# Optimization experiments

Hardware: AMD Instinct MI355X
Metric: run time of the kernel (lower is better)

The kernel has to match this reference:

```python
import jax, jax.numpy as jnp
import numpy as np

DIM = 768
N_IMGS = 1024
N_PATCH = 196
GRID = int(np.sqrt(N_PATCH))  # 14
B = 64


def setup_inputs() -> dict:
    key = jax.random.key(0)
    ks = jax.random.split(key, 12)
    x = jax.random.normal(ks[0], (B, N_PATCH, DIM), dtype=jnp.float32)
    mask = jnp.ones((B, N_PATCH), dtype=jnp.bool_)
    img_ids = jax.random.randint(ks[1], (B,), 0, N_IMGS, dtype=jnp.int32)
    eps = jax.random.normal(ks[2], (B, 2, N_PATCH), dtype=jnp.float32)
    s = 0.02
    Wq = jax.random.normal(ks[3], (DIM, DIM), dtype=jnp.float32) * s
    bq = jnp.zeros((DIM,), dtype=jnp.float32)
    Wk = jax.random.normal(ks[4], (DIM, DIM), dtype=jnp.float32) * s
    bk = jnp.zeros((DIM,), dtype=jnp.float32)
    Wv = jax.random.normal(ks[5], (DIM, DIM), dtype=jnp.float32) * s
    bv = jnp.zeros((DIM,), dtype=jnp.float32)
    # per-image Gaussian location params: means in [0, GRID-1], small positive stds
    avgs = jax.random.uniform(ks[6], (N_IMGS, 2, N_PATCH), dtype=jnp.float32) * (GRID - 1)
    std_devs = jax.random.uniform(ks[7], (N_IMGS, 2, N_PATCH), dtype=jnp.float32) * 1.5 + 0.1
    return {"x": x, "mask": mask, "img_ids": img_ids, "eps": eps,
            "Wq": Wq, "bq": bq, "Wk": Wk, "bk": bk, "Wv": Wv, "bv": bv,
            "avgs": avgs, "std_devs": std_devs}


def reference(x, mask, img_ids, eps, Wq, bq, Wk, bk, Wv, bv, avgs, std_devs):
    # projections: (B,S,D)
    q = jnp.einsum('bsd,ed->bse', x, Wq) + bq
    k = jnp.einsum('bsd,ed->bse', x, Wk) + bk
    v = jnp.einsum('bsd,ed->bse', x, Wv) + bv

    # sample per-query key coordinates: torch.normal(mean, std) == mean + std * eps
    mu = avgs[img_ids]        # (B,2,S)
    sd = std_devs[img_ids]    # (B,2,S)
    coord = mu + sd * eps     # (B,2,S)
    kx, ky = coord[:, 0], coord[:, 1]           # each (B,S)
    kx1, kx2 = jnp.ceil(kx), jnp.floor(kx)
    ky1, ky2 = jnp.ceil(ky), jnp.floor(ky)

    # 4 interpolation-corner flat indices per query: grid*y + x  -> (B,S,4)
    idx = jnp.stack([GRID * ky1 + kx1,
                     GRID * ky1 + kx2,
                     GRID * ky2 + kx1,
                     GRID * ky2 + kx2], axis=-1)
    idx = jnp.clip(idx, 0, N_PATCH - 1).astype(jnp.int32)

    bidx = jnp.arange(idx.shape[0])[:, None, None]  # (B,1,1)
    sampled_k = k[bidx, idx]  # (B,S,4,D)
    sampled_v = v[bidx, idx]  # (B,S,4,D)

    # softmax over the 4 sampled keys (elementwise per feature), weighted sum of values
    w = jax.nn.softmax(q[:, :, None, :] * sampled_k, axis=2)  # (B,S,4,D)
    out = jnp.sum(w * sampled_v, axis=2)                      # (B,S,D)
    return out
```

## Files before the change

### kernel.cpp

```cpp
#include <hip/hip_runtime.h>
#include <hip/hip_bf16.h>

typedef _Float16 f16;
typedef f16 f16x4 __attribute__((ext_vector_type(4)));
typedef f16 f16x8 __attribute__((ext_vector_type(8)));
typedef float f32x4 __attribute__((ext_vector_type(4)));

#define DIM   768
#define NP    196
#define BATCH 64
#define MROWS (BATCH * NP)
#define NCOLS (3 * DIM)
#define GRIDF 14.0f

#define NX4   (MROWS * DIM / 4)
#define NW4   (DIM * DIM / 4)
#define NB4   (NCOLS / 4)
#define NCVTA (NX4 + 3 * NW4 + NB4)

__global__ __launch_bounds__(256) void convert_inputs(
    const float* __restrict__ x,
    const float* __restrict__ Wq, const float* __restrict__ Wk, const float* __restrict__ Wv,
    const float* __restrict__ bq, const float* __restrict__ bk, const float* __restrict__ bv,
    f16* __restrict__ x_h, f16* __restrict__ W_h, float* __restrict__ bias_all) {
  int i = blockIdx.x * 256 + threadIdx.x;
  if (i >= NCVTA) return;
  if (i < NX4 + 3 * NW4) {
    const float* src;
    f16* dst;
    int j;
    if (i < NX4) { src = x; dst = x_h; j = i; }
    else {
      j = i - NX4;
      if (j < NW4)          { src = Wq; dst = W_h; }
      else if (j < 2 * NW4) { src = Wk; dst = W_h + DIM * DIM;     j -= NW4; }
      else                  { src = Wv; dst = W_h + 2 * DIM * DIM; j -= 2 * NW4; }
    }
    float4 v = ((const float4*)src)[j];
    f16x4 h;
    h[0] = (f16)v.x; h[1] = (f16)v.y; h[2] = (f16)v.z; h[3] = (f16)v.w;
    ((f16x4*)dst)[j] = h;
  } else {
    int j = i - (NX4 + 3 * NW4);
    float4 v = (j < 192) ? ((const float4*)bq)[j]
             : (j < 384) ? ((const float4*)bk)[j - 192]
                         : ((const float4*)bv)[j - 384];
    ((float4*)bias_all)[j] = v;
  }
}

#define BM 128
#define BN 128
#define BK 64
#define NT (DIM / BK)

__device__ __forceinline__ void gl_lds16(const f16* g, f16* l) {
  __builtin_amdgcn_global_load_lds(
      (const __attribute__((address_space(1))) void*)g,
      (__attribute__((address_space(3))) void*)l, 16, 0, 0);
}

#define MFMA16(acc_, av, bv) acc_ = __builtin_amdgcn_mfma_f32_16x16x32_f16(av, bv, acc_, 0, 0, 0)
#define BAR    __builtin_amdgcn_s_barrier()
#define LGKM8  asm volatile("s_waitcnt lgkmcnt(8)" ::: "memory")
#define LGKM0  asm volatile("s_waitcnt lgkmcnt(0)" ::: "memory")
#define VMCNT8 asm volatile("s_waitcnt vmcnt(8)" ::: "memory")
#define VMCNT0 asm volatile("s_waitcnt vmcnt(0)" ::: "memory")

#define sAoff(buf) ((buf) * (BM * BK))
#define sBoff(buf) (2 * BM * BK + (buf) * (BN * BK))

__global__ __launch_bounds__(256, 2) void gemm_qkv(
    const f16* __restrict__ A, const f16* __restrict__ W,
    const float* __restrict__ bias_all, f16* __restrict__ C) {
  __shared__ __align__(16) f16 lds[4 * BM * BK];

  const int t    = threadIdx.x;
  const int lane = t & 63;
  const int wid  = t >> 6;
  const int wr   = wid >> 1;
  const int wc   = wid & 1;

  const int nwg = 98 * 18, qq = nwg / 8, rr = nwg % 8;
  const int xcd = blockIdx.x & 7, seq = blockIdx.x >> 3;
  const int logical = (xcd < rr ? xcd * (qq + 1) : rr * (qq + 1) + (xcd - rr) * qq) + seq;
  const int bm0 = (logical / 18) * BM;
  const int bn0 = (logical % 18) * BN;

  const int srow  = t >> 3;
  const int sslot = t & 7;
  const int gcol  = 8 * (sslot ^ (srow & 7));
  const int lds_off = srow * BK + sslot * 8;
  const f16* gAr = A + (size_t)(bm0 + srow) * DIM + gcol;
  const f16* gBr = W + (size_t)(bn0 + srow) * DIM + gcol;

#define STAGE_A(kt) do {                                             \
    const f16* _g = gAr + (kt) * BK;                                 \
    f16* _l = &lds[sAoff((kt) & 1) + lds_off];                       \
    gl_lds16(_g,                       _l);                          \
    gl_lds16(_g + (size_t)32  * DIM,   _l + 32  * BK);               \
    gl_lds16(_g + (size_t)64  * DIM,   _l + 64  * BK);               \
    gl_lds16(_g + (size_t)96  * DIM,   _l + 96  * BK);               \
  } while (0)

#define STAGE_B(kt) do {                                             \
    const f16* _g = gBr + (kt) * BK;                                 \
    f16* _l = &lds[sBoff((kt) & 1) + lds_off];                       \
    gl_lds16(_g,                       _l);                          \
    gl_lds16(_g + (size_t)32  * DIM,   _l + 32  * BK);               \
    gl_lds16(_g + (size_t)64  * DIM,   _l + 64  * BK);               \
    gl_lds16(_g + (size_t)96  * DIM,   _l + 96  * BK);               \
  } while (0)

  const int rl = lane & 15;
  const int kg = lane >> 4;
  const int s7 = lane & 7;
  const int slot0 = ((0 * 4 + kg) ^ s7) * 8;
  const int slot1 = ((1 * 4 + kg) ^ s7) * 8;
  const int aBase = (wr * 64 + rl) * BK;
  const int bBase = (wc * 64 + rl) * BK;

  f32x4 acc[4][4] = {};
  f16x8 afr[4][2], bfr[4][2];

#define LDAB_KH0(buf) do {                                                              \
    _Pragma("unroll") for (int ni = 0; ni < 4; ++ni)                                    \
      bfr[ni][0] = *(const f16x8*)&lds[sBoff(buf) + bBase + ni * 16 * BK + slot0];      \
    _Pragma("unroll") for (int mi = 0; mi < 4; ++mi)                                    \
      afr[mi][0] = *(const f16x8*)&lds[sAoff(buf) + aBase + mi * 16 * BK + slot0];      \
    } while (0)

#define LDAB_KH1(buf) do {                                                              \
    _Pragma("unroll") for (int ni = 0; ni < 4; ++ni)                                    \
      bfr[ni][1] = *(const f16x8*)&lds[sBoff(buf) + bBase + ni * 16 * BK + slot1];      \
    _Pragma("unroll") for (int mi = 0; mi < 4; ++mi)                                    \
      afr[mi][1] = *(const f16x8*)&lds[sAoff(buf) + aBase + mi * 16 * BK + slot1];      \
    } while (0)

#define MMA_KH(kh) do {                                                          \
    __builtin_amdgcn_s_setprio(1);                                               \
    _Pragma("unroll") for (int ni = 0; ni < 4; ++ni)                             \
      _Pragma("unroll") for (int mi = 0; mi < 4; ++mi)                           \
        MFMA16(acc[mi][ni], bfr[ni][kh], afr[mi][kh]);                           \
    __builtin_amdgcn_s_setprio(0); } while (0)

  STAGE_A(0); STAGE_B(0);
  STAGE_A(1); STAGE_B(1);
  VMCNT8;
  BAR;

  for (int kt = 0; kt < NT; ++kt) {
    const int b = kt & 1;
    const bool more = (kt + 2 < NT);
    LDAB_KH0(b);
    LDAB_KH1(b);
    LGKM8;
    MMA_KH(0);
    LGKM0; BAR;
    if (more) { STAGE_A(kt + 2); STAGE_B(kt + 2); }
    MMA_KH(1);
    if (more) { VMCNT8; } else { VMCNT0; }
    BAR;
  }

  {
    const int eRow0 = wr * 64 + rl;
    const int nq0   = wc * 64 + 4 * kg;
#pragma unroll
    for (int ni = 0; ni < 4; ++ni) {
      const int nloc = nq0 + ni * 16;
      const float4 b4 = *(const float4*)&bias_all[bn0 + nloc];
#pragma unroll
      for (int mi = 0; mi < 4; ++mi) {
        const int e = eRow0 + mi * 16;
        f16x4 h;
        h[0] = (f16)(acc[mi][ni][0] + b4.x);
        h[1] = (f16)(acc[mi][ni][1] + b4.y);
        h[2] = (f16)(acc[mi][ni][2] + b4.z);
        h[3] = (f16)(acc[mi][ni][3] + b4.w);
        *(f16x4*)&lds[e * 128 + (nloc ^ ((e & 7) << 3))] = h;
      }
    }
    LGKM0; BAR;
    const int rrow = t >> 4;
    const int rchk = t & 15;
#pragma unroll
    for (int p = 0; p < 8; ++p) {
      const int row = p * 16 + rrow;
      f16x8 vdat = *(const f16x8*)&lds[row * 128 + ((rchk * 8) ^ ((row & 7) << 3))];
      *(f16x8*)&C[(size_t)(bm0 + row) * NCOLS + bn0 + rchk * 8] = vdat;
    }
  }
}

__global__ __launch_bounds__(256) void attend(
    const f16* __restrict__ qkv,
    const int* __restrict__ img_ids, const float* __restrict__ eps,
    const float* __restrict__ avgs, const float* __restrict__ stds,
    float* __restrict__ out) {
  const int lane = threadIdx.x & 63;
  const int wid  = threadIdx.x >> 6;
  const int logical = (blockIdx.x & 7) * 392 + (blockIdx.x >> 3);
  const int gw = logical * 4 + wid;
  const int b = gw / NP;
  const int s = gw - b * NP;

  const int img = img_ids[b];
  const float ex = eps[(b * 2 + 0) * NP + s];
  const float ey = eps[(b * 2 + 1) * NP + s];
  const float mux = avgs[(img * 2 + 0) * NP + s];
  const float muy = avgs[(img * 2 + 1) * NP + s];
  const float sdx = stds[(img * 2 + 0) * NP + s];
  const float sdy = stds[(img * 2 + 1) * NP + s];

  const float kx = fmaf(sdx, ex, mux);
  const float ky = fmaf(sdy, ey, muy);
  const float kx1 = ceilf(kx), kx2 = floorf(kx);
  const float ky1 = ceilf(ky), ky2 = floorf(ky);

  int idx[4];
  idx[0] = (int)fminf(fmaxf(GRIDF * ky1 + kx1, 0.0f), 195.0f);
  idx[1] = (int)fminf(fmaxf(GRIDF * ky1 + kx2, 0.0f), 195.0f);
  idx[2] = (int)fminf(fmaxf(GRIDF * ky2 + kx1, 0.0f), 195.0f);
  idx[3] = (int)fminf(fmaxf(GRIDF * ky2 + kx2, 0.0f), 195.0f);

  const f16* qrow = qkv + (size_t)gw * NCOLS;
  const f16* base = qkv + (size_t)(b * NP) * NCOLS;
  const f16* k0p = base + (size_t)idx[0] * NCOLS + DIM;
  const f16* k1p = base + (size_t)idx[1] * NCOLS + DIM;
  const f16* k2p = base + (size_t)idx[2] * NCOLS + DIM;
  const f16* k3p = base + (size_t)idx[3] * NCOLS + DIM;
  const f16* v0p = k0p + DIM;
  const f16* v1p = k1p + DIM;
  const f16* v2p = k2p + DIM;
  const f16* v3p = k3p + DIM;
  float* orow = out + (size_t)gw * DIM;

#pragma unroll
  for (int seg = 0; seg < 3; ++seg) {
    const int e0 = seg * 256 + lane * 4;
    f16x4 qv  = *(const f16x4*)(qrow + e0);
    f16x4 kv0 = *(const f16x4*)(k0p + e0);
    f16x4 kv1 = *(const f16x4*)(k1p + e0);
    f16x4 kv2 = *(const f16x4*)(k2p + e0);
    f16x4 kv3 = *(const f16x4*)(k3p + e0);
    f16x4 vv0 = *(const f16x4*)(v0p + e0);
    f16x4 vv1 = *(const f16x4*)(v1p + e0);
    f16x4 vv2 = *(const f16x4*)(v2p + e0);
    f16x4 vv3 = *(const f16x4*)(v3p + e0);
    float4 o;
    float* op = &o.x;
#pragma unroll
    for (int c = 0; c < 4; ++c) {
      const float q = (float)qv[c];
      const float s0 = q * (float)kv0[c];
      const float s1 = q * (float)kv1[c];
      const float s2 = q * (float)kv2[c];
      const float s3 = q * (float)kv3[c];
      const float mx = fmaxf(fmaxf(s0, s1), fmaxf(s2, s3));
      const float w0 = __expf(s0 - mx);
      const float w1 = __expf(s1 - mx);
      const float w2 = __expf(s2 - mx);
      const float w3 = __expf(s3 - mx);
      const float den = w0 + w1 + w2 + w3;
      const float num = w0 * (float)vv0[c] + w1 * (float)vv1[c] +
                        w2 * (float)vv2[c] + w3 * (float)vv3[c];
      op[c] = num / den;
    }
    *(float4*)(orow + e0) = o;
  }
}

extern "C" void kernel_launch(void* const* d_in, const int* in_sizes, int n_in,
                              void* d_out, int out_size, void* d_ws, size_t ws_size,
                              hipStream_t stream) {
  const float* x       = (const float*)d_in[0];
  const int*   img_ids = (const int*)d_in[2];
  const float* eps     = (const float*)d_in[3];
  const float* Wq      = (const float*)d_in[4];
  const float* bq      = (const float*)d_in[5];
  const float* Wk      = (const float*)d_in[6];
  const float* bk      = (const float*)d_in[7];
  const float* Wv      = (const float*)d_in[8];
  const float* bv      = (const float*)d_in[9];
  const float* avgs    = (const float*)d_in[10];
  const float* stds    = (const float*)d_in[11];
  float* out = (float*)d_out;

  char* ws = (char*)d_ws;
  const size_t XH_BYTES = (size_t)MROWS * DIM * 2;
  const size_t WH_BYTES = (size_t)NCOLS * DIM * 2;
  const size_t BI_BYTES = (size_t)NCOLS * 4;
  f16*   x_h      = (f16*)ws;
  f16*   W_h      = (f16*)(ws + XH_BYTES);
  float* bias_all = (float*)(ws + XH_BYTES + WH_BYTES);
  f16*   qkv      = (f16*)(ws + XH_BYTES + WH_BYTES + BI_BYTES);

  {
    int grid = (NCVTA + 255) / 256;
    convert_inputs<<<grid, 256, 0, stream>>>(x, Wq, Wk, Wv, bq, bk, bv, x_h, W_h, bias_all);
  }
  {
    gemm_qkv<<<1764, 256, 0, stream>>>(x_h, W_h, bias_all, qkv);
  }
  {
    int grid = MROWS / 4;
    attend<<<grid, 256, 0, stream>>>(qkv, img_ids, eps, avgs, stds, out);
  }
}
```

Measured before the change: 83.44 us.

## Enlarge QKV GEMM tiles to 224x256 with 8-wave workgroups

Raises the GEMM block tile from 128x128 to 224x256 (M divides 12544 evenly into 56 row tiles, N into 9 column tiles) and moves to 512-thread workgroups with a 2x4 wave grid, each wave computing 7x4 MFMA tiles. The grid drops from 1764 to 504 blocks, laid out so each XCD gets 63 contiguous tiles. Larger tiles raise arithmetic intensity and cut redundant global loads of A and W. The trade-off is more register pressure (28 accumulators per wave), more LDS, an idle dummy-load path for the extra A-staging threads, and a modest tail with 504 blocks on 256 CUs.

```diff
diff --git a/kernel.cpp b/kernel.cpp
--- a/kernel.cpp
+++ b/kernel.cpp
@@ -49,10 +49,17 @@
   }
 }
 
-#define BM 128
-#define BN 128
+#define BM 224
+#define BN 256
 #define BK 64
 #define NT (DIM / BK)
+
+#define SA_SZ   (BM * BK)
+#define SB_SZ   (BN * BK)
+#define sAoff(buf) ((buf) * SA_SZ)
+#define sBoff(buf) (2 * SA_SZ + (buf) * SB_SZ)
+#define SCRAPF  (2 * SA_SZ + 2 * SB_SZ)
+#define LDS_F16 (SCRAPF + 512)
 
 __device__ __forceinline__ void gl_lds16(const f16* g, f16* l) {
   __builtin_amdgcn_global_load_lds(
@@ -61,55 +68,60 @@
 }
 
 #define MFMA16(acc_, av, bv) acc_ = __builtin_amdgcn_mfma_f32_16x16x32_f16(av, bv, acc_, 0, 0, 0)
-#define BAR    __builtin_amdgcn_s_barrier()
-#define LGKM8  asm volatile("s_waitcnt lgkmcnt(8)" ::: "memory")
-#define LGKM0  asm volatile("s_waitcnt lgkmcnt(0)" ::: "memory")
-#define VMCNT8 asm volatile("s_waitcnt vmcnt(8)" ::: "memory")
-#define VMCNT0 asm volatile("s_waitcnt vmcnt(0)" ::: "memory")
-
-#define sAoff(buf) ((buf) * (BM * BK))
-#define sBoff(buf) (2 * BM * BK + (buf) * (BN * BK))
-
-__global__ __launch_bounds__(256, 2) void gemm_qkv(
+#define BAR     __builtin_amdgcn_s_barrier()
+#define LGKM11  asm volatile("s_waitcnt lgkmcnt(11)" ::: "memory")
+#define LGKM0   asm volatile("s_waitcnt lgkmcnt(0)" ::: "memory")
+#define VMCNT8  asm volatile("s_waitcnt vmcnt(8)" ::: "memory")
+#define VMCNT0  asm volatile("s_waitcnt vmcnt(0)" ::: "memory")
+
+__global__ __launch_bounds__(512, 2) void gemm_qkv(
     const f16* __restrict__ A, const f16* __restrict__ W,
     const float* __restrict__ bias_all, f16* __restrict__ C) {
-  __shared__ __align__(16) f16 lds[4 * BM * BK];
+  __shared__ __align__(16) f16 lds[LDS_F16];
 
   const int t    = threadIdx.x;
   const int lane = t & 63;
   const int wid  = t >> 6;
-  const int wr   = wid >> 1;
-  const int wc   = wid & 1;
-
-  const int nwg = 98 * 18, qq = nwg / 8, rr = nwg % 8;
+  const int wr   = wid >> 2;
+  const int wc   = wid & 3;
+
   const int xcd = blockIdx.x & 7, seq = blockIdx.x >> 3;
-  const int logical = (xcd < rr ? xcd * (qq + 1) : rr * (qq + 1) + (xcd - rr) * qq) + seq;
-  const int bm0 = (logical / 18) * BM;
-  const int bn0 = (logical % 18) * BN;
-
-  const int srow  = t >> 3;
-  const int sslot = t & 7;
-  const int gcol  = 8 * (sslot ^ (srow & 7));
-  const int lds_off = srow * BK + sslot * 8;
-  const f16* gAr = A + (size_t)(bm0 + srow) * DIM + gcol;
-  const f16* gBr = W + (size_t)(bn0 + srow) * DIM + gcol;
-
-#define STAGE_A(kt) do {                                             \
-    const f16* _g = gAr + (kt) * BK;                                 \
-    f16* _l = &lds[sAoff((kt) & 1) + lds_off];                       \
-    gl_lds16(_g,                       _l);                          \
-    gl_lds16(_g + (size_t)32  * DIM,   _l + 32  * BK);               \
-    gl_lds16(_g + (size_t)64  * DIM,   _l + 64  * BK);               \
-    gl_lds16(_g + (size_t)96  * DIM,   _l + 96  * BK);               \
+  const int logical = xcd * 63 + seq;
+  const int bm0 = (logical / 9) * BM;
+  const int bn0 = (logical % 9) * BN;
+
+  const bool realA = (t < 448);
+  const int arow  = realA ? (t >> 3) : 0;
+  const int aslot = t & 7;
+  const int agcol = 8 * (aslot ^ (arow & 7));
+  const f16* gA_base = realA ? (A + (size_t)(bm0 + arow) * DIM + agcol)
+                             : (W + (size_t)(bn0 + lane) * DIM);
+  const int aoff_rel   = realA ? (arow * BK + aslot * 8) : (lane * 8);
+  const size_t a_gstr  = realA ? (size_t)56 * DIM : 0;
+  const int    a_lstr  = realA ? 56 * BK : 0;
+
+#define STAGE_A(kt) do {                                                       \
+    const f16* _g = gA_base + (kt) * BK;                                       \
+    f16* _l = &lds[(realA ? sAoff((kt) & 1) : SCRAPF) + aoff_rel];             \
+    gl_lds16(_g,              _l);                                             \
+    gl_lds16(_g + a_gstr,     _l + a_lstr);                                    \
+    gl_lds16(_g + 2 * a_gstr, _l + 2 * a_lstr);                                \
+    gl_lds16(_g + 3 * a_gstr, _l + 3 * a_lstr);                                \
   } while (0)
 
-#define STAGE_B(kt) do {                                             \
-    const f16* _g = gBr + (kt) * BK;                                 \
-    f16* _l = &lds[sBoff((kt) & 1) + lds_off];                       \
-    gl_lds16(_g,                       _l);                          \
-    gl_lds16(_g + (size_t)32  * DIM,   _l + 32  * BK);               \
-    gl_lds16(_g + (size_t)64  * DIM,   _l + 64  * BK);               \
-    gl_lds16(_g + (size_t)96  * DIM,   _l + 96  * BK);               \
+  const int brow  = t >> 3;
+  const int bslot = t & 7;
+  const int bgcol = 8 * (bslot ^ (brow & 7));
+  const f16* gB_base = W + (size_t)(bn0 + brow) * DIM + bgcol;
+  const int boff = brow * BK + bslot * 8;
+
+#define STAGE_B(kt) do {                                                       \
+    const f16* _g = gB_base + (kt) * BK;                                       \
+    f16* _l = &lds[sBoff((kt) & 1) + boff];                                    \
+    gl_lds16(_g,                      _l);                                     \
+    gl_lds16(_g + (size_t)64  * DIM,  _l + 64  * BK);                          \
+    gl_lds16(_g + (size_t)128 * DIM,  _l + 128 * BK);                          \
+    gl_lds16(_g + (size_t)192 * DIM,  _l + 192 * BK);                          \
   } while (0)
 
   const int rl = lane & 15;
@@ -117,30 +129,30 @@
   const int s7 = lane & 7;
   const int slot0 = ((0 * 4 + kg) ^ s7) * 8;
   const int slot1 = ((1 * 4 + kg) ^ s7) * 8;
-  const int aBase = (wr * 64 + rl) * BK;
+  const int aBase = (wr * 112 + rl) * BK;
   const int bBase = (wc * 64 + rl) * BK;
 
-  f32x4 acc[4][4] = {};
-  f16x8 afr[4][2], bfr[4][2];
+  f32x4 acc[7][4] = {};
+  f16x8 afr[7][2], bfr[4][2];
 
 #define LDAB_KH0(buf) do {                                                              \
     _Pragma("unroll") for (int ni = 0; ni < 4; ++ni)                                    \
       bfr[ni][0] = *(const f16x8*)&lds[sBoff(buf) + bBase + ni * 16 * BK + slot0];      \
-    _Pragma("unroll") for (int mi = 0; mi < 4; ++mi)                                    \
+    _Pragma("unroll") for (int mi = 0; mi < 7; ++mi)                                    \
       afr[mi][0] = *(const f16x8*)&lds[sAoff(buf) + aBase + mi * 16 * BK + slot0];      \
     } while (0)
 
 #define LDAB_KH1(buf) do {                                                              \
     _Pragma("unroll") for (int ni = 0; ni < 4; ++ni)                                    \
       bfr[ni][1] = *(const f16x8*)&lds[sBoff(buf) + bBase + ni * 16 * BK + slot1];      \
-    _Pragma("unroll") for (int mi = 0; mi < 4; ++mi)                                    \
+    _Pragma("unroll") for (int mi = 0; mi < 7; ++mi)                                    \
       afr[mi][1] = *(const f16x8*)&lds[sAoff(buf) + aBase + mi * 16 * BK + slot1];      \
     } while (0)
 
 #define MMA_KH(kh) do {                                                          \
     __builtin_amdgcn_s_setprio(1);                                               \
     _Pragma("unroll") for (int ni = 0; ni < 4; ++ni)                             \
-      _Pragma("unroll") for (int mi = 0; mi < 4; ++mi)                           \
+      _Pragma("unroll") for (int mi = 0; mi < 7; ++mi)                           \
         MFMA16(acc[mi][ni], bfr[ni][kh], afr[mi][kh]);                           \
     __builtin_amdgcn_s_setprio(0); } while (0)
 
@@ -154,7 +166,7 @@
     const bool more = (kt + 2 < NT);
     LDAB_KH0(b);
     LDAB_KH1(b);
-    LGKM8;
+    LGKM11;
     MMA_KH(0);
     LGKM0; BAR;
     if (more) { STAGE_A(kt + 2); STAGE_B(kt + 2); }
@@ -164,30 +176,30 @@
   }
 
   {
-    const int eRow0 = wr * 64 + rl;
+    const int eRow0 = wr * 112 + rl;
     const int nq0   = wc * 64 + 4 * kg;
 #pragma unroll
     for (int ni = 0; ni < 4; ++ni) {
       const int nloc = nq0 + ni * 16;
       const float4 b4 = *(const float4*)&bias_all[bn0 + nloc];
 #pragma unroll
-      for (int mi = 0; mi < 4; ++mi) {
+      for (int mi = 0; mi < 7; ++mi) {
         const int e = eRow0 + mi * 16;
         f16x4 h;
         h[0] = (f16)(acc[mi][ni][0] + b4.x);
         h[1] = (f16)(acc[mi][ni][1] + b4.y);
         h[2] = (f16)(acc[mi][ni][2] + b4.z);
         h[3] = (f16)(acc[mi][ni][3] + b4.w);
-        *(f16x4*)&lds[e * 128 + (nloc ^ ((e & 7) << 3))] = h;
+        *(f16x4*)&lds[e * 256 + (nloc ^ ((e & 7) << 3))] = h;
       }
     }
     LGKM0; BAR;
-    const int rrow = t >> 4;
-    const int rchk = t & 15;
-#pragma unroll
-    for (int p = 0; p < 8; ++p) {
+    const int rrow = t >> 5;
+    const int rchk = t & 31;
+#pragma unroll
+    for (int p = 0; p < 14; ++p) {
       const int row = p * 16 + rrow;
-      f16x8 vdat = *(const f16x8*)&lds[row * 128 + ((rchk * 8) ^ ((row & 7) << 3))];
+      f16x8 vdat = *(const f16x8*)&lds[row * 256 + ((rchk * 8) ^ ((row & 7) << 3))];
       *(f16x8*)&C[(size_t)(bm0 + row) * NCOLS + bn0 + rchk * 8] = vdat;
     }
   }
@@ -301,7 +313,7 @@
     convert_inputs<<<grid, 256, 0, stream>>>(x, Wq, Wk, Wv, bq, bk, bv, x_h, W_h, bias_all);
   }
   {
-    gemm_qkv<<<1764, 256, 0, stream>>>(x_h, W_h, bias_all, qkv);
+    gemm_qkv<<<504, 512, 0, stream>>>(x_h, W_h, bias_all, qkv);
   }
   {
     int grid = MROWS / 4;
```

Measured after the change: 86.31 us. +3.4%, slower.
